# Optimization experiments

Hardware: AMD Instinct MI355X
Metric: run time of the kernel (lower is better)

## Reference

```python
import jax, jax.numpy as jnp
import numpy as np

HIDDEN = 2048
N_HEADS = 16
N_KV = 4
HEAD_DIM = 128
EPS = 1e-6
B = 8
L = 1024
PREFIX = 256
SUFFIX = L - PREFIX
N_COMPACT = PREFIX + B * SUFFIX  # 6400
T_FULL = B * L                   # 8192
ROPE_THETA = 10000.0


def _radix_indices():
    # full position (b, p) -> compact index
    scatter = np.empty(T_FULL, dtype=np.int64)
    for b in range(B):
        scatter[b * L: b * L + PREFIX] = np.arange(PREFIX)
        scatter[b * L + PREFIX: (b + 1) * L] = PREFIX + b * SUFFIX + np.arange(SUFFIX)
    # compact index -> first full occurrence
    fold = np.empty(N_COMPACT, dtype=np.int64)
    fold[:PREFIX] = np.arange(PREFIX)
    for b in range(B):
        fold[PREFIX + b * SUFFIX: PREFIX + (b + 1) * SUFFIX] = b * L + PREFIX + np.arange(SUFFIX)
    return scatter, fold


def setup_inputs() -> dict:
    key = jax.random.key(0)
    ks = jax.random.split(key, 8)
    scatter_np, fold_np = _radix_indices()
    # per-compact-token positions for RoPE
    pos = np.empty(N_COMPACT, dtype=np.float32)
    pos[:PREFIX] = np.arange(PREFIX)
    for b in range(B):
        pos[PREFIX + b * SUFFIX: PREFIX + (b + 1) * SUFFIX] = PREFIX + np.arange(SUFFIX)
    inv_freq = ROPE_THETA ** (-np.arange(HEAD_DIM // 2, dtype=np.float32) / (HEAD_DIM // 2))
    freqs = pos[:, None] * inv_freq[None, :]  # [N_c, 64]
    s = 0.02
    return {
        "hidden_states": jax.random.normal(ks[0], (N_COMPACT, HIDDEN), jnp.float32),
        "cos": jnp.asarray(np.cos(freqs), jnp.float32),
        "sin": jnp.asarray(np.sin(freqs), jnp.float32),
        "cu_seq_lengths": jnp.arange(B + 1, dtype=jnp.int32) * L,
        "max_seq_len": L,
        "fold_gather": jnp.asarray(fold_np),
        "scatter_indices": jnp.asarray(scatter_np),
        "wq": jax.random.normal(ks[1], (HIDDEN, N_HEADS * HEAD_DIM), jnp.float32) * s,
        "wk": jax.random.normal(ks[2], (HIDDEN, N_KV * HEAD_DIM), jnp.float32) * s,
        "wv": jax.random.normal(ks[3], (HIDDEN, N_KV * HEAD_DIM), jnp.float32) * s,
        "wo": jax.random.normal(ks[4], (N_HEADS * HEAD_DIM, HIDDEN), jnp.float32) * s,
        "q_norm_w": jnp.ones((HEAD_DIM,), jnp.float32),
        "k_norm_w": jnp.ones((HEAD_DIM,), jnp.float32),
    }


def _rmsnorm(x, w):
    xf = x.astype(jnp.float32)
    var = jnp.mean(xf * xf, axis=-1, keepdims=True)
    return (w * (xf * jax.lax.rsqrt(var + EPS))).astype(x.dtype)


def _rope(x, cos, sin):
    # x: [N, H, D]; cos/sin: [N, D/2]
    half = cos.shape[-1]
    x1, x2 = x[..., :half], x[..., half:2 * half]
    c, s = cos[:, None, :], sin[:, None, :]
    return jnp.concatenate([x1 * c - x2 * s, x1 * s + x2 * c], axis=-1)


def reference(hidden_states, cos, sin, cu_seq_lengths, max_seq_len,
              fold_gather, scatter_indices, wq, wk, wv, wo, q_norm_w, k_norm_w):
    N = hidden_states.shape[0]
    q = (hidden_states @ wq).reshape(N, N_HEADS, HEAD_DIM)
    k = (hidden_states @ wk).reshape(N, N_KV, HEAD_DIM)
    v = (hidden_states @ wv).reshape(N, N_KV, HEAD_DIM)
    q = _rope(_rmsnorm(q, q_norm_w), cos, sin)
    k = _rope(_rmsnorm(k, k_norm_w), cos, sin)
    # radix scatter: expand compact tokens to full varlen token stream
    qf = q[scatter_indices].reshape(B, L, N_HEADS, HEAD_DIM)
    kf = k[scatter_indices].reshape(B, L, N_KV, HEAD_DIM)
    vf = v[scatter_indices].reshape(B, L, N_KV, HEAD_DIM)
    group = N_HEADS // N_KV
    kf = jnp.repeat(kf, group, axis=2)
    vf = jnp.repeat(vf, group, axis=2)
    scale = HEAD_DIM ** -0.5
    scores = jnp.einsum('bqhd,bkhd->bhqk', qf, kf) * scale
    causal = jnp.tril(jnp.ones((L, L), dtype=bool))
    scores = jnp.where(causal[None, None], scores, jnp.finfo(scores.dtype).min)
    probs = jax.nn.softmax(scores, axis=-1)
    out = jnp.einsum('bhqk,bkhd->bqhd', probs, vf).reshape(T_FULL, N_HEADS * HEAD_DIM)
    # radix fold: gather back to compact tokens
    out_compact = out[fold_gather]
    return out_compact @ wo
```

## Files before the change

kernel.cpp:

```cpp
#include <hip/hip_runtime.h>
#include <hip/hip_bf16.h>

typedef __bf16 bf16;
typedef __bf16 bf16x8 __attribute__((ext_vector_type(8)));
typedef float f32x4 __attribute__((ext_vector_type(4)));

#define HID 2048
#define NHEADS 16
#define NKV 4
#define HD 128
#define NC 6400
#define KVW (NKV * HD)

__device__ __forceinline__ void async_cp16(const bf16* src, bf16* dst_lds) {
  __builtin_amdgcn_global_load_lds(
      (const __attribute__((address_space(1))) void*)src,
      (__attribute__((address_space(3))) void*)dst_lds, 16, 0, 0);
}

__global__ __launch_bounds__(256) void k_cvt(const float* __restrict__ in,
                                             bf16* __restrict__ out) {
  size_t i = ((size_t)blockIdx.x * 256 + threadIdx.x) * 8;
  f32x4 a = *(const f32x4*)(in + i);
  f32x4 b = *(const f32x4*)(in + i + 4);
  bf16x8 t;
  for (int j = 0; j < 4; j++) {
    t[j] = (bf16)a[j];
    t[j + 4] = (bf16)b[j];
  }
  *(bf16x8*)(out + i) = t;
}

__global__ __launch_bounds__(256) void k_transpose(const float* __restrict__ in,
                                                   bf16* __restrict__ out,
                                                   int R, int C) {
  __shared__ bf16 tile[32][33];
  int bc = blockIdx.x * 32, br = blockIdx.y * 32;
  int tx = threadIdx.x & 31, ty = threadIdx.x >> 5;
  for (int i = 0; i < 32; i += 8)
    tile[ty + i][tx] = (bf16)in[(size_t)(br + ty + i) * C + bc + tx];
  __syncthreads();
  for (int i = 0; i < 32; i += 8)
    out[(size_t)(bc + ty + i) * R + br + tx] = tile[tx][ty + i];
}

__device__ __forceinline__ void gemm256_core(
    const bf16* __restrict__ A, const bf16* __restrict__ Bt, int m0, int nloc,
    int K, bf16* AsB, bf16* BsB, f32x4 (&acc)[2][4][4]) {
  const int tid = threadIdx.x;
  const int lane = tid & 63, wave = tid >> 6;
  const int l15 = lane & 15, quad = lane >> 4;
  const int wr = wave >> 2, wc = wave & 3;
  const int r0A = wr * 128 + l15;
  const int r0B = wc * 64 + l15;
  const int colOff0 = (quad * 8) ^ ((l15 & 7) << 3);
  const int colOff1 = (32 + quad * 8) ^ ((l15 & 7) << 3);
  const int c0 = tid, c1 = 512 + tid;
  const size_t offS0 =
      (size_t)(c0 >> 3) * K + (((((c0 & 7) << 4) ^ (((c0 >> 3) & 7) << 4))) >> 1);
  const size_t offS1 =
      (size_t)(c1 >> 3) * K + (((((c1 & 7) << 4) ^ (((c1 >> 3) & 7) << 4))) >> 1);
  const int dstW0 = wave * 512;
  const int dstW1 = 4096 + wave * 512;
  const bf16* Abase = A + (size_t)m0 * K;
  const bf16* Bbase = Bt + (size_t)nloc * K;
  const int KM = K - 1;

#define STAGE(gb, lds, dbuf, h, kc)                             \
  do {                                                          \
    const bf16* _s = (gb) + (size_t)(h) * 128 * K + (kc);       \
    bf16* _d = (lds) + (dbuf) * 16384 + (h) * 8192;             \
    async_cp16(_s + offS0, _d + dstW0);                         \
    async_cp16(_s + offS1, _d + dstW1);                         \
  } while (0)

#define LDA(dbuf, mh)                                           \
  do {                                                          \
    _Pragma("unroll") for (int i = 0; i < 4; i++) {             \
      int r = r0A + (mh) * 64 + i * 16;                         \
      const bf16* p = AsB + (dbuf) * 16384 + r * 64;            \
      a[i][0] = *(const bf16x8*)(p + colOff0);                  \
      a[i][1] = *(const bf16x8*)(p + colOff1);                  \
    }                                                           \
  } while (0)

#define LDB(dbuf, nh, bb)                                       \
  do {                                                          \
    _Pragma("unroll") for (int j = 0; j < 2; j++) {             \
      int r = r0B + (nh) * 32 + j * 16;                         \
      const bf16* p = BsB + (dbuf) * 16384 + r * 64;            \
      bb[j][0] = *(const bf16x8*)(p + colOff0);                 \
      bb[j][1] = *(const bf16x8*)(p + colOff1);                 \
    }                                                           \
  } while (0)

#define MFMAQ(mh, nh, bb)                                                    \
  do {                                                                       \
    __builtin_amdgcn_s_setprio(1);                                           \
    _Pragma("unroll") for (int i = 0; i < 4; i++)                            \
        _Pragma("unroll") for (int j = 0; j < 2; j++) {                      \
      acc[mh][i][(nh) * 2 + j] = __builtin_amdgcn_mfma_f32_16x16x32_bf16(    \
          a[i][0], bb[j][0], acc[mh][i][(nh) * 2 + j], 0, 0, 0);             \
      acc[mh][i][(nh) * 2 + j] = __builtin_amdgcn_mfma_f32_16x16x32_bf16(    \
          a[i][1], bb[j][1], acc[mh][i][(nh) * 2 + j], 0, 0, 0);             \
    }                                                                        \
    __builtin_amdgcn_s_setprio(0);                                           \
  } while (0)

  STAGE(Abase, AsB, 0, 0, 0);
  STAGE(Abase, AsB, 0, 1, 0);
  STAGE(Bbase, BsB, 0, 0, 0);
  STAGE(Bbase, BsB, 0, 1, 0);
  STAGE(Bbase, BsB, 1, 0, 64);
  STAGE(Bbase, BsB, 1, 1, 64);
  asm volatile("s_waitcnt vmcnt(4)" ::: "memory");
  __builtin_amdgcn_s_barrier();
  __builtin_amdgcn_sched_barrier(0);

  bf16x8 a[4][2], b0[2][2], b1[2][2];

  const int NIT = K >> 7;
#pragma unroll 1
  for (int it = 0; it < NIT; ++it) {
    const int kb = it << 7;
    LDA(0, 0);
    LDB(0, 0, b0);
    STAGE(Abase, AsB, 1, 0, (kb + 64) & KM);
    asm volatile("s_waitcnt lgkmcnt(8)");
    __builtin_amdgcn_s_barrier();
    asm volatile("s_waitcnt lgkmcnt(0)" ::: "memory");
    MFMAQ(0, 0, b0);
    __builtin_amdgcn_s_barrier();
    __builtin_amdgcn_sched_barrier(0);
    LDB(0, 1, b1);
    STAGE(Abase, AsB, 1, 1, (kb + 64) & KM);
    __builtin_amdgcn_s_barrier();
    asm volatile("s_waitcnt lgkmcnt(0)" ::: "memory");
    MFMAQ(0, 1, b1);
    __builtin_amdgcn_s_barrier();
    __builtin_amdgcn_sched_barrier(0);
    LDA(0, 1);
    STAGE(Bbase, BsB, 0, 0, (kb + 128) & KM);
    __builtin_amdgcn_s_barrier();
    asm volatile("s_waitcnt lgkmcnt(0)" ::: "memory");
    MFMAQ(1, 0, b0);
    __builtin_amdgcn_s_barrier();
    __builtin_amdgcn_sched_barrier(0);
    STAGE(Bbase, BsB, 0, 1, (kb + 128) & KM);
    __builtin_amdgcn_s_barrier();
    MFMAQ(1, 1, b1);
    asm volatile("s_waitcnt vmcnt(4)" ::: "memory");
    __builtin_amdgcn_s_barrier();
    __builtin_amdgcn_sched_barrier(0);
    LDA(1, 0);
    LDB(1, 0, b0);
    STAGE(Abase, AsB, 0, 0, (kb + 128) & KM);
    asm volatile("s_waitcnt lgkmcnt(8)");
    __builtin_amdgcn_s_barrier();
    asm volatile("s_waitcnt lgkmcnt(0)" ::: "memory");
    MFMAQ(0, 0, b0);
    __builtin_amdgcn_s_barrier();
    __builtin_amdgcn_sched_barrier(0);
    LDB(1, 1, b1);
    STAGE(Abase, AsB, 0, 1, (kb + 128) & KM);
    __builtin_amdgcn_s_barrier();
    asm volatile("s_waitcnt lgkmcnt(0)" ::: "memory");
    MFMAQ(0, 1, b1);
    __builtin_amdgcn_s_barrier();
    __builtin_amdgcn_sched_barrier(0);
    LDA(1, 1);
    STAGE(Bbase, BsB, 1, 0, (kb + 192) & KM);
    __builtin_amdgcn_s_barrier();
    asm volatile("s_waitcnt lgkmcnt(0)" ::: "memory");
    MFMAQ(1, 0, b0);
    __builtin_amdgcn_s_barrier();
    __builtin_amdgcn_sched_barrier(0);
    STAGE(Bbase, BsB, 1, 1, (kb + 192) & KM);
    __builtin_amdgcn_s_barrier();
    MFMAQ(1, 1, b1);
    asm volatile("s_waitcnt vmcnt(4)" ::: "memory");
    __builtin_amdgcn_s_barrier();
    __builtin_amdgcn_sched_barrier(0);
  }
#undef STAGE
#undef LDA
#undef LDB
#undef MFMAQ
}

__global__ __launch_bounds__(512, 2) void k_proj(const bf16* __restrict__ A,
                                                 const bf16* __restrict__ wqT,
                                                 const bf16* __restrict__ wkT,
                                                 const bf16* __restrict__ wvT,
                                                 bf16* __restrict__ qb,
                                                 bf16* __restrict__ kb,
                                                 bf16* __restrict__ vtb) {
  __shared__ __align__(16) bf16 As[2][256][64];
  __shared__ __align__(16) bf16 Bs[2][256][64];
  int n0 = blockIdx.x * 256, m0 = blockIdx.y * 256;

  const bf16* bt;
  int nloc, outsel;
  if (n0 < HID) {
    bt = wqT; nloc = n0; outsel = 0;
  } else if (n0 < HID + KVW) {
    bt = wkT; nloc = n0 - HID; outsel = 1;
  } else {
    bt = wvT; nloc = n0 - HID - KVW; outsel = 2;
  }

  const f32x4 fz = {0.0f, 0.0f, 0.0f, 0.0f};
  f32x4 acc[2][4][4];
#pragma unroll
  for (int mh = 0; mh < 2; mh++)
#pragma unroll
    for (int i = 0; i < 4; i++)
#pragma unroll
      for (int j = 0; j < 4; j++) acc[mh][i][j] = fz;

  gemm256_core(A, bt, m0, nloc, HID, &As[0][0][0], &Bs[0][0][0], acc);

  int tid = threadIdx.x, lane = tid & 63, wave = tid >> 6;
  int l15 = lane & 15, quad = lane >> 4;
  int wr = wave >> 2, wc = wave & 3;
#pragma unroll
  for (int mh = 0; mh < 2; mh++)
#pragma unroll
    for (int i = 0; i < 4; i++)
#pragma unroll
      for (int nj = 0; nj < 4; nj++)
#pragma unroll
        for (int r = 0; r < 4; r++) {
          int row = m0 + wr * 128 + mh * 64 + i * 16 + quad * 4 + r;
          int col = nloc + wc * 64 + nj * 16 + l15;
          float v = acc[mh][i][nj][r];
          if (outsel == 0)
            qb[(size_t)row * HID + col] = (bf16)v;
          else if (outsel == 1)
            kb[(size_t)row * KVW + col] = (bf16)v;
          else
            vtb[(size_t)col * NC + row] = (bf16)v;
        }
}

__global__ __launch_bounds__(512, 2) void k_gemm_out(const bf16* __restrict__ A,
                                                     const bf16* __restrict__ Bt,
                                                     float* __restrict__ C,
                                                     int M, int N, int K) {
  __shared__ __align__(16) bf16 As[2][256][64];
  __shared__ __align__(16) bf16 Bs[2][256][64];
  int n0 = blockIdx.x * 256, m0 = blockIdx.y * 256;

  const f32x4 fz = {0.0f, 0.0f, 0.0f, 0.0f};
  f32x4 acc[2][4][4];
#pragma unroll
  for (int mh = 0; mh < 2; mh++)
#pragma unroll
    for (int i = 0; i < 4; i++)
#pragma unroll
      for (int j = 0; j < 4; j++) acc[mh][i][j] = fz;

  gemm256_core(A, Bt, m0, n0, K, &As[0][0][0], &Bs[0][0][0], acc);

  int tid = threadIdx.x, lane = tid & 63, wave = tid >> 6;
  int l15 = lane & 15, quad = lane >> 4;
  int wr = wave >> 2, wc = wave & 3;
#pragma unroll
  for (int mh = 0; mh < 2; mh++)
#pragma unroll
    for (int i = 0; i < 4; i++)
#pragma unroll
      for (int nj = 0; nj < 4; nj++)
#pragma unroll
        for (int r = 0; r < 4; r++) {
          int row = m0 + wr * 128 + mh * 64 + i * 16 + quad * 4 + r;
          int col = n0 + wc * 64 + nj * 16 + l15;
          C[(size_t)row * N + col] = acc[mh][i][nj][r];
        }
}

__global__ __launch_bounds__(256) void k_normrope(bf16* __restrict__ q,
                                                  bf16* __restrict__ k,
                                                  const float* __restrict__ cs,
                                                  const float* __restrict__ sn,
                                                  const float* __restrict__ qw,
                                                  const float* __restrict__ kw) {
  int pair = blockIdx.x * 4 + (threadIdx.x >> 6);
  int lane = threadIdx.x & 63;
  int n = pair / 20, hh = pair % 20;
  bf16* base;
  const float* w;
  if (hh < 16) {
    base = q + (size_t)n * HID + hh * HD;
    w = qw;
  } else {
    base = k + (size_t)n * KVW + (hh - 16) * HD;
    w = kw;
  }
  float x1 = (float)base[lane], x2 = (float)base[lane + 64];
  float ss = x1 * x1 + x2 * x2;
  for (int o = 32; o; o >>= 1) ss += __shfl_xor(ss, o);
  float inv = rsqrtf(ss * (1.0f / 128.0f) + 1e-6f);
  float x1n = x1 * inv * w[lane];
  float x2n = x2 * inv * w[lane + 64];
  float c = cs[(size_t)n * 64 + lane];
  float s = sn[(size_t)n * 64 + lane];
  base[lane] = (bf16)(x1n * c - x2n * s);
  base[lane + 64] = (bf16)(x1n * s + x2n * c);
}

__global__ __launch_bounds__(256) void k_attn(const bf16* __restrict__ qb,
                                              const bf16* __restrict__ kb,
                                              const bf16* __restrict__ vt,
                                              bf16* __restrict__ ob) {
  int qt = blockIdx.x;
  int h = blockIdx.y;
  int kh = h >> 2;
  int tid = threadIdx.x;
  int lane = tid & 63, wave = tid >> 6;
  int l15 = lane & 15, quad = lane >> 4;

  int b, p0, nbase;
  if (qt < 4) {
    b = 0;
    p0 = qt * 64;
    nbase = qt * 64;
  } else {
    int t = qt - 4;
    b = t / 12;
    int ti = t - b * 12;
    p0 = 256 + ti * 64;
    nbase = 256 + b * 768 + ti * 64;
  }

  __shared__ __align__(16) bf16 Ks[64][136];
  __shared__ __align__(16) bf16 Vs[128][72];
  __shared__ __align__(16) bf16 Ps[4][16][72];

  bf16x8 aq[4];
  {
    const bf16* qp =
        qb + (size_t)(nbase + wave * 16 + l15) * HID + h * HD + quad * 8;
    for (int ks = 0; ks < 4; ks++) aq[ks] = *(const bf16x8*)(qp + ks * 32);
  }
  int qpos[4];
  for (int r = 0; r < 4; r++) qpos[r] = p0 + wave * 16 + quad * 4 + r;

  const f32x4 fz = {0.0f, 0.0f, 0.0f, 0.0f};
  f32x4 oacc[8];
  for (int i = 0; i < 8; i++) oacc[i] = fz;
  float mrow[4], lrow[4];
  for (int r = 0; r < 4; r++) {
    mrow[r] = -3.0e38f;
    lrow[r] = 0.0f;
  }
  const float scale = 0.08838834764831845f;

  int nkt = p0 / 64 + 1;
  for (int kt = 0; kt < nkt; kt++) {
    int kpos0 = kt * 64;
    int kbase = (kpos0 < 256) ? kpos0 : 256 + b * 768 + (kpos0 - 256);
    __syncthreads();
    for (int s = 0; s < 4; s++) {
      int c = tid + 256 * s;
      int key = c >> 4, dc = c & 15;
      *(uint4*)&Ks[key][dc * 8] =
          *(const uint4*)(kb + (size_t)(kbase + key) * KVW + kh * HD + dc * 8);
    }
    for (int s = 0; s < 4; s++) {
      int c = tid + 256 * s;
      int d = c >> 3, kc = c & 7;
      *(uint4*)&Vs[d][kc * 8] =
          *(const uint4*)(vt + (size_t)(kh * HD + d) * NC + kbase + kc * 8);
    }
    __syncthreads();

    bool diag = (kt == nkt - 1);
    float sv[4][4];
    for (int nt = 0; nt < 4; nt++) {
      f32x4 z = fz;
      for (int ks = 0; ks < 4; ks++) {
        bf16x8 kf = *(const bf16x8*)&Ks[nt * 16 + l15][ks * 32 + quad * 8];
        z = __builtin_amdgcn_mfma_f32_16x16x32_bf16(aq[ks], kf, z, 0, 0, 0);
      }
      int kpos = kpos0 + nt * 16 + l15;
      for (int r = 0; r < 4; r++) {
        float v = z[r] * scale;
        if (diag && kpos > qpos[r]) v = -1.0e30f;
        sv[nt][r] = v;
      }
    }
    float alpha[4];
    for (int r = 0; r < 4; r++) {
      float mx = fmaxf(fmaxf(sv[0][r], sv[1][r]), fmaxf(sv[2][r], sv[3][r]));
      for (int o = 1; o < 16; o <<= 1) mx = fmaxf(mx, __shfl_xor(mx, o));
      float mnew = fmaxf(mrow[r], mx);
      alpha[r] = __expf(mrow[r] - mnew);
      mrow[r] = mnew;
      float ps = 0.0f;
      for (int nt = 0; nt < 4; nt++) {
        float p = __expf(sv[nt][r] - mnew);
        sv[nt][r] = p;
        ps += p;
      }
      for (int o = 1; o < 16; o <<= 1) ps += __shfl_xor(ps, o);
      lrow[r] = lrow[r] * alpha[r] + ps;
    }
    for (int i = 0; i < 8; i++)
      for (int r = 0; r < 4; r++) oacc[i][r] *= alpha[r];

    for (int nt = 0; nt < 4; nt++)
      for (int r = 0; r < 4; r++)
        Ps[wave][quad * 4 + r][nt * 16 + l15] = (bf16)sv[nt][r];
    __syncthreads();
    bf16x8 pa[2];
    for (int ks = 0; ks < 2; ks++)
      pa[ks] = *(const bf16x8*)&Ps[wave][l15][ks * 32 + quad * 8];
    for (int dt = 0; dt < 8; dt++)
      for (int ks = 0; ks < 2; ks++) {
        bf16x8 vf = *(const bf16x8*)&Vs[dt * 16 + l15][ks * 32 + quad * 8];
        oacc[dt] =
            __builtin_amdgcn_mfma_f32_16x16x32_bf16(pa[ks], vf, oacc[dt], 0, 0, 0);
      }
  }
  for (int r = 0; r < 4; r++) {
    float il = 1.0f / lrow[r];
    bf16* op = ob + (size_t)(nbase + wave * 16 + quad * 4 + r) * HID + h * HD;
    for (int dt = 0; dt < 8; dt++) op[dt * 16 + l15] = (bf16)(oacc[dt][r] * il);
  }
}

extern "C" void kernel_launch(void* const* d_in, const int* in_sizes, int n_in,
                              void* d_out, int out_size, void* d_ws,
                              size_t ws_size, hipStream_t stream) {
  const float* hs = (const float*)d_in[0];
  const float* cs = (const float*)d_in[1];
  const float* sn = (const float*)d_in[2];
  const float* wq = (const float*)d_in[7];
  const float* wk = (const float*)d_in[8];
  const float* wv = (const float*)d_in[9];
  const float* wo = (const float*)d_in[10];
  const float* qnw = (const float*)d_in[11];
  const float* knw = (const float*)d_in[12];
  float* out = (float*)d_out;

  bf16* hsb = (bf16*)d_out;
  bf16* wqT = hsb + (size_t)NC * HID;
  bf16* wkT = wqT + (size_t)HID * HID;
  bf16* wvT = wkT + (size_t)KVW * HID;
  bf16* qb  = (bf16*)d_in[0];
  bf16* ab  = qb + (size_t)NC * HID;
  bf16* woT = qb;
  bf16* kb  = (bf16*)d_ws;
  bf16* vtb = kb + (size_t)NC * KVW;

  k_cvt<<<dim3(NC * HID / (256 * 8)), 256, 0, stream>>>(hs, hsb);
  k_transpose<<<dim3(HID / 32, HID / 32), 256, 0, stream>>>(wq, wqT, HID, HID);
  k_transpose<<<dim3(KVW / 32, HID / 32), 256, 0, stream>>>(wk, wkT, HID, KVW);
  k_transpose<<<dim3(KVW / 32, HID / 32), 256, 0, stream>>>(wv, wvT, HID, KVW);

  k_proj<<<dim3((HID + 2 * KVW) / 256, NC / 256), 512, 0, stream>>>(
      hsb, wqT, wkT, wvT, qb, kb, vtb);

  k_normrope<<<dim3(NC * 20 / 4), 256, 0, stream>>>(qb, kb, cs, sn, qnw, knw);

  k_attn<<<dim3(100, NHEADS), 256, 0, stream>>>(qb, kb, vtb, ab);

  k_transpose<<<dim3(HID / 32, HID / 32), 256, 0, stream>>>(wo, woT, HID, HID);

  k_gemm_out<<<dim3(HID / 256, NC / 256), 512, 0, stream>>>(ab, woT, out, NC, HID, HID);
}
```

Before: 512.1 us.

## Re-pipeline GEMM staging, add XCD block swizzle, LDS-transposed V output

Moves A-tile staging earlier in the GEMM main loop, prefetching the next A half during the previous MFMA phase, and removes the sched_barriers so the compiler can interleave more freely. Adds an XCD-aware workgroup remap to both GEMM kernels so neighbouring tiles share L2 on the same XCD. The V projection output, written transposed, now goes through a swizzled LDS tile and is stored with 16-byte vector writes instead of strided scalar stores. Changing the vmcnt/lgkmcnt waits raises the risk of LDS hazards, and LDS reuse in the epilogue adds extra barriers.

```diff
diff --git a/kernel.cpp b/kernel.cpp
--- a/kernel.cpp
+++ b/kernel.cpp
@@ -2,6 +2,7 @@
 #include <hip/hip_bf16.h>
 
 typedef __bf16 bf16;
+typedef __bf16 bf16x4 __attribute__((ext_vector_type(4)));
 typedef __bf16 bf16x8 __attribute__((ext_vector_type(8)));
 typedef float f32x4 __attribute__((ext_vector_type(4)));
 
@@ -16,6 +17,17 @@
   __builtin_amdgcn_global_load_lds(
       (const __attribute__((address_space(1))) void*)src,
       (__attribute__((address_space(3))) void*)dst_lds, 16, 0, 0);
+}
+
+__device__ __forceinline__ void xcd_swizzle(int& bx, int& by) {
+  int nx = gridDim.x;
+  int nwg = nx * gridDim.y;
+  int id = by * nx + bx;
+  int q = nwg >> 3, r = nwg & 7;
+  int xcd = id & 7, idx = id >> 3;
+  int nid = (xcd < r ? xcd * (q + 1) : r * (q + 1) + (xcd - r) * q) + idx;
+  bx = nid % nx;
+  by = nid / nx;
 }
 
 __global__ __launch_bounds__(256) void k_cvt(const float* __restrict__ in,
@@ -55,11 +67,9 @@
   const int r0B = wc * 64 + l15;
   const int colOff0 = (quad * 8) ^ ((l15 & 7) << 3);
   const int colOff1 = (32 + quad * 8) ^ ((l15 & 7) << 3);
-  const int c0 = tid, c1 = 512 + tid;
   const size_t offS0 =
-      (size_t)(c0 >> 3) * K + (((((c0 & 7) << 4) ^ (((c0 >> 3) & 7) << 4))) >> 1);
-  const size_t offS1 =
-      (size_t)(c1 >> 3) * K + (((((c1 & 7) << 4) ^ (((c1 >> 3) & 7) << 4))) >> 1);
+      (size_t)(tid >> 3) * K + ((((tid & 7) ^ ((tid >> 3) & 7)) << 4) >> 1);
+  const size_t offS1 = offS0 + (size_t)64 * K;
   const int dstW0 = wave * 512;
   const int dstW1 = 4096 + wave * 512;
   const bf16* Abase = A + (size_t)m0 * K;
@@ -113,9 +123,9 @@
   STAGE(Bbase, BsB, 0, 1, 0);
   STAGE(Bbase, BsB, 1, 0, 64);
   STAGE(Bbase, BsB, 1, 1, 64);
-  asm volatile("s_waitcnt vmcnt(4)" ::: "memory");
+  STAGE(Abase, AsB, 1, 0, 64);
+  asm volatile("s_waitcnt vmcnt(6)" ::: "memory");
   __builtin_amdgcn_s_barrier();
-  __builtin_amdgcn_sched_barrier(0);
 
   bf16x8 a[4][2], b0[2][2], b1[2][2];
 
@@ -125,33 +135,29 @@
     const int kb = it << 7;
     LDA(0, 0);
     LDB(0, 0, b0);
-    STAGE(Abase, AsB, 1, 0, (kb + 64) & KM);
+    STAGE(Abase, AsB, 1, 1, (kb + 64) & KM);
     asm volatile("s_waitcnt lgkmcnt(8)");
     __builtin_amdgcn_s_barrier();
     asm volatile("s_waitcnt lgkmcnt(0)" ::: "memory");
     MFMAQ(0, 0, b0);
     __builtin_amdgcn_s_barrier();
-    __builtin_amdgcn_sched_barrier(0);
     LDB(0, 1, b1);
-    STAGE(Abase, AsB, 1, 1, (kb + 64) & KM);
     __builtin_amdgcn_s_barrier();
     asm volatile("s_waitcnt lgkmcnt(0)" ::: "memory");
     MFMAQ(0, 1, b1);
     __builtin_amdgcn_s_barrier();
-    __builtin_amdgcn_sched_barrier(0);
     LDA(0, 1);
     STAGE(Bbase, BsB, 0, 0, (kb + 128) & KM);
     __builtin_amdgcn_s_barrier();
     asm volatile("s_waitcnt lgkmcnt(0)" ::: "memory");
     MFMAQ(1, 0, b0);
     __builtin_amdgcn_s_barrier();
-    __builtin_amdgcn_sched_barrier(0);
     STAGE(Bbase, BsB, 0, 1, (kb + 128) & KM);
     __builtin_amdgcn_s_barrier();
+    asm volatile("s_waitcnt lgkmcnt(0)" ::: "memory");
     MFMAQ(1, 1, b1);
     asm volatile("s_waitcnt vmcnt(4)" ::: "memory");
     __builtin_amdgcn_s_barrier();
-    __builtin_amdgcn_sched_barrier(0);
     LDA(1, 0);
     LDB(1, 0, b0);
     STAGE(Abase, AsB, 0, 0, (kb + 128) & KM);
@@ -160,27 +166,25 @@
     asm volatile("s_waitcnt lgkmcnt(0)" ::: "memory");
     MFMAQ(0, 0, b0);
     __builtin_amdgcn_s_barrier();
-    __builtin_amdgcn_sched_barrier(0);
     LDB(1, 1, b1);
     STAGE(Abase, AsB, 0, 1, (kb + 128) & KM);
     __builtin_amdgcn_s_barrier();
     asm volatile("s_waitcnt lgkmcnt(0)" ::: "memory");
     MFMAQ(0, 1, b1);
     __builtin_amdgcn_s_barrier();
-    __builtin_amdgcn_sched_barrier(0);
     LDA(1, 1);
     STAGE(Bbase, BsB, 1, 0, (kb + 192) & KM);
     __builtin_amdgcn_s_barrier();
     asm volatile("s_waitcnt lgkmcnt(0)" ::: "memory");
     MFMAQ(1, 0, b0);
     __builtin_amdgcn_s_barrier();
-    __builtin_amdgcn_sched_barrier(0);
     STAGE(Bbase, BsB, 1, 1, (kb + 192) & KM);
-    __builtin_amdgcn_s_barrier();
+    STAGE(Abase, AsB, 1, 0, (kb + 192) & KM);
+    __builtin_amdgcn_s_barrier();
+    asm volatile("s_waitcnt lgkmcnt(0)" ::: "memory");
     MFMAQ(1, 1, b1);
-    asm volatile("s_waitcnt vmcnt(4)" ::: "memory");
-    __builtin_amdgcn_s_barrier();
-    __builtin_amdgcn_sched_barrier(0);
+    asm volatile("s_waitcnt vmcnt(6)" ::: "memory");
+    __builtin_amdgcn_s_barrier();
   }
 #undef STAGE
 #undef LDA
@@ -195,9 +199,10 @@
                                                  bf16* __restrict__ qb,
                                                  bf16* __restrict__ kb,
                                                  bf16* __restrict__ vtb) {
-  __shared__ __align__(16) bf16 As[2][256][64];
-  __shared__ __align__(16) bf16 Bs[2][256][64];
-  int n0 = blockIdx.x * 256, m0 = blockIdx.y * 256;
+  __shared__ __align__(16) bf16 smem[2][2][256][64];
+  int bx = blockIdx.x, by = blockIdx.y;
+  xcd_swizzle(bx, by);
+  int n0 = bx * 256, m0 = by * 256;
 
   const bf16* bt;
   int nloc, outsel;
@@ -218,38 +223,70 @@
 #pragma unroll
       for (int j = 0; j < 4; j++) acc[mh][i][j] = fz;
 
-  gemm256_core(A, bt, m0, nloc, HID, &As[0][0][0], &Bs[0][0][0], acc);
+  gemm256_core(A, bt, m0, nloc, HID, &smem[0][0][0][0], &smem[1][0][0][0], acc);
 
   int tid = threadIdx.x, lane = tid & 63, wave = tid >> 6;
   int l15 = lane & 15, quad = lane >> 4;
   int wr = wave >> 2, wc = wave & 3;
-#pragma unroll
-  for (int mh = 0; mh < 2; mh++)
-#pragma unroll
-    for (int i = 0; i < 4; i++)
-#pragma unroll
-      for (int nj = 0; nj < 4; nj++)
-#pragma unroll
-        for (int r = 0; r < 4; r++) {
-          int row = m0 + wr * 128 + mh * 64 + i * 16 + quad * 4 + r;
-          int col = nloc + wc * 64 + nj * 16 + l15;
-          float v = acc[mh][i][nj][r];
-          if (outsel == 0)
-            qb[(size_t)row * HID + col] = (bf16)v;
-          else if (outsel == 1)
-            kb[(size_t)row * KVW + col] = (bf16)v;
-          else
-            vtb[(size_t)col * NC + row] = (bf16)v;
+
+  if (outsel == 2) {
+    asm volatile("s_waitcnt vmcnt(0)" ::: "memory");
+    __syncthreads();
+    bf16* sm = &smem[0][0][0][0];
+#pragma unroll
+    for (int mh = 0; mh < 2; mh++)
+#pragma unroll
+      for (int i = 0; i < 4; i++)
+#pragma unroll
+        for (int nj = 0; nj < 4; nj++) {
+          int col = wc * 64 + nj * 16 + l15;
+          int row = wr * 128 + mh * 64 + i * 16 + quad * 4;
+          int idx = col * 256 + ((row + ((col & 7) << 3)) & 255);
+          bf16x4 v4 = {(bf16)acc[mh][i][nj][0], (bf16)acc[mh][i][nj][1],
+                       (bf16)acc[mh][i][nj][2], (bf16)acc[mh][i][nj][3]};
+          *(bf16x4*)&sm[idx] = v4;
         }
+    __syncthreads();
+#pragma unroll
+    for (int p = 0; p < 4; p++) {
+      int cc = p * 64 + (tid >> 3);
+      int h = tid & 7;
+#pragma unroll
+      for (int j = 0; j < 4; j++) {
+        int row8 = h * 32 + j * 8;
+        bf16x8 v =
+            *(const bf16x8*)&sm[cc * 256 + ((row8 + ((cc & 7) << 3)) & 255)];
+        *(bf16x8*)(vtb + (size_t)(nloc + cc) * NC + m0 + row8) = v;
+      }
+    }
+  } else {
+#pragma unroll
+    for (int mh = 0; mh < 2; mh++)
+#pragma unroll
+      for (int i = 0; i < 4; i++)
+#pragma unroll
+        for (int nj = 0; nj < 4; nj++)
+#pragma unroll
+          for (int r = 0; r < 4; r++) {
+            int row = m0 + wr * 128 + mh * 64 + i * 16 + quad * 4 + r;
+            int col = nloc + wc * 64 + nj * 16 + l15;
+            float v = acc[mh][i][nj][r];
+            if (outsel == 0)
+              qb[(size_t)row * HID + col] = (bf16)v;
+            else
+              kb[(size_t)row * KVW + col] = (bf16)v;
+          }
+  }
 }
 
 __global__ __launch_bounds__(512, 2) void k_gemm_out(const bf16* __restrict__ A,
                                                      const bf16* __restrict__ Bt,
                                                      float* __restrict__ C,
                                                      int M, int N, int K) {
-  __shared__ __align__(16) bf16 As[2][256][64];
-  __shared__ __align__(16) bf16 Bs[2][256][64];
-  int n0 = blockIdx.x * 256, m0 = blockIdx.y * 256;
+  __shared__ __align__(16) bf16 smem[2][2][256][64];
+  int bx = blockIdx.x, by = blockIdx.y;
+  xcd_swizzle(bx, by);
+  int n0 = bx * 256, m0 = by * 256;
 
   const f32x4 fz = {0.0f, 0.0f, 0.0f, 0.0f};
   f32x4 acc[2][4][4];
@@ -260,7 +297,7 @@
 #pragma unroll
       for (int j = 0; j < 4; j++) acc[mh][i][j] = fz;
 
-  gemm256_core(A, Bt, m0, n0, K, &As[0][0][0], &Bs[0][0][0], acc);
+  gemm256_core(A, Bt, m0, n0, K, &smem[0][0][0][0], &smem[1][0][0][0], acc);
 
   int tid = threadIdx.x, lane = tid & 63, wave = tid >> 6;
   int l15 = lane & 15, quad = lane >> 4;
```

New measurement: 472.2 us. 1.08x faster.
